# Optimization experiments

Hardware: AMD Instinct MI355X
Metric: run time of the kernel (lower is better)

The kernel has to match this reference:

```python
import jax, jax.numpy as jnp
import numpy as np

DIM = 1024
DIM_INNER = 1536  # int(1024 * 1.5)


def _log_g(x):
    # log of g(x) = where(x>=0, x+0.5, sigmoid(x)) computed stably in log-space
    return jnp.where(x >= 0.0, jnp.log(jnp.maximum(x, 0.0) + 0.5), -jax.nn.softplus(-x))


def _heinsen_scan_log(log_coefficients, log_values):
    # parallel associative scan in log space over the sequence axis (axis=1)
    a_star = jnp.cumsum(log_coefficients, axis=1)
    log_h0_plus_b_star = jax.lax.cumlogsumexp(log_values - a_star, axis=1)
    return jnp.exp(a_star + log_h0_plus_b_star)


def _forward_gru(x, W_hg, W_out):
    # x: [b, s, dim] -> hidden/gate: [b, s, dim_inner]
    hg = jnp.einsum('bsd,ed->bse', x, W_hg)
    hidden, gate = jnp.split(hg, 2, axis=-1)
    log_coefficients = -jax.nn.softplus(gate)      # log(1 - z)
    log_z = -jax.nn.softplus(-gate)                # log z
    log_values = log_z + _log_g(hidden)
    out = _heinsen_scan_log(log_coefficients, log_values)  # [b, s, dim_inner]
    return jnp.einsum('bse,de->bsd', out, W_out)


def setup_inputs() -> dict:
    key = jax.random.key(0)
    k1, k2, k3 = jax.random.split(key, 3)
    x = jax.random.normal(k1, (4, 4096, DIM), dtype=jnp.float32)
    W_hg = jax.random.normal(k2, (2 * DIM_INNER, DIM), dtype=jnp.float32) * (DIM ** -0.5)
    W_out = jax.random.normal(k3, (DIM, DIM_INNER), dtype=jnp.float32) * (DIM_INNER ** -0.5)
    return {"x": x, "W_hg": W_hg, "W_out": W_out}


def reference(x, W_hg, W_out):
    out_forward = _forward_gru(x, W_hg, W_out)
    # bidirectional=True: run on time-flipped input and add (module does NOT flip back)
    out_backward = _forward_gru(jnp.flip(x, axis=1), W_hg, W_out)
    return out_forward + out_backward
```

## Files before the change

kernel.cpp:

```cpp
#include <hip/hip_runtime.h>
#include <hip/hip_fp16.h>
#include <cstdint>
#include <cstddef>

#define B_ 4
#define S_ 4096
#define D_ 1024
#define E_ 1536
#define M_ (B_*S_)
#define BE_ (B_*E_)
#define C_ 32
#define L_ (S_/C_)

typedef short bf16x8 __attribute__((ext_vector_type(8)));
typedef float f32x4 __attribute__((ext_vector_type(4)));

__device__ __forceinline__ unsigned short f2b(float f) {
  union { float f; unsigned int i; } x; x.f = f;
  unsigned int r = x.i + 0x7FFFu + ((x.i >> 16) & 1u);
  return (unsigned short)(r >> 16);
}
__device__ __forceinline__ float h2f(unsigned short u) { return __half2float(__ushort_as_half(u)); }
__device__ __forceinline__ unsigned int packcv(float c, float v) {
  return (unsigned int)__half_as_ushort(__float2half_rn(c)) |
         ((unsigned int)__half_as_ushort(__float2half_rn(v)) << 16);
}

__global__ __launch_bounds__(256) void cvt_bf16(const float* __restrict__ src,
                                                unsigned short* __restrict__ dst) {
  const int i = blockIdx.x * 256 + threadIdx.x;
  float4 f = ((const float4*)src)[i];
  ushort4 u; u.x = f2b(f.x); u.y = f2b(f.y); u.z = f2b(f.z); u.w = f2b(f.w);
  ((ushort4*)dst)[i] = u;
}

__global__ __launch_bounds__(256) void gemm1_mfma(const unsigned short* __restrict__ Xb,
                                                  const unsigned short* __restrict__ Wb,
                                                  unsigned int* __restrict__ CV) {
  __shared__ unsigned short lA[128 * 32];
  __shared__ unsigned short lB[128 * 32];
  const int t = threadIdx.x;
  const int m0 = blockIdx.x * 128;
  const int n0 = blockIdx.y * 64;
  const int wv = t >> 6, lane = t & 63;
  const int wm = wv >> 1, we = wv & 1;
  const int lm = lane & 15, kg = lane >> 4;
  const int r1 = t >> 2, q1 = t & 3;
  const int r2 = r1 + 64;
  const int gb1 = (r1 < 64) ? (n0 + r1) : (E_ + n0 + r1 - 64);
  const int gb2 = (r2 < 64) ? (n0 + r2) : (E_ + n0 + r2 - 64);

  const f32x4 z4 = {0.f, 0.f, 0.f, 0.f};
  f32x4 ah[4][2], ag[4][2];
#pragma unroll
  for (int i = 0; i < 4; ++i)
#pragma unroll
    for (int j = 0; j < 2; ++j) { ah[i][j] = z4; ag[i][j] = z4; }

  for (int k0 = 0; k0 < D_; k0 += 32) {
    *(uint4*)(lA + (size_t)r1 * 32 + q1 * 8) = *(const uint4*)(Xb + (size_t)(m0 + r1) * D_ + k0 + q1 * 8);
    *(uint4*)(lA + (size_t)r2 * 32 + q1 * 8) = *(const uint4*)(Xb + (size_t)(m0 + r2) * D_ + k0 + q1 * 8);
    *(uint4*)(lB + (size_t)r1 * 32 + q1 * 8) = *(const uint4*)(Wb + (size_t)gb1 * D_ + k0 + q1 * 8);
    *(uint4*)(lB + (size_t)r2 * 32 + q1 * 8) = *(const uint4*)(Wb + (size_t)gb2 * D_ + k0 + q1 * 8);
    __syncthreads();
    bf16x8 af[4], bh[2], bg[2];
#pragma unroll
    for (int mt = 0; mt < 4; ++mt)
      af[mt] = *(const bf16x8*)(lA + (size_t)(wm * 64 + mt * 16 + lm) * 32 + kg * 8);
#pragma unroll
    for (int et = 0; et < 2; ++et) {
      bh[et] = *(const bf16x8*)(lB + (size_t)(we * 32 + et * 16 + lm) * 32 + kg * 8);
      bg[et] = *(const bf16x8*)(lB + (size_t)(64 + we * 32 + et * 16 + lm) * 32 + kg * 8);
    }
#pragma unroll
    for (int mt = 0; mt < 4; ++mt)
#pragma unroll
      for (int et = 0; et < 2; ++et) {
        ah[mt][et] = __builtin_amdgcn_mfma_f32_16x16x32_bf16(af[mt], bh[et], ah[mt][et], 0, 0, 0);
        ag[mt][et] = __builtin_amdgcn_mfma_f32_16x16x32_bf16(af[mt], bg[et], ag[mt][et], 0, 0, 0);
      }
    __syncthreads();
  }
#pragma unroll
  for (int mt = 0; mt < 4; ++mt)
#pragma unroll
    for (int et = 0; et < 2; ++et) {
      const int e = n0 + we * 32 + et * 16 + lm;
#pragma unroll
      for (int r = 0; r < 4; ++r) {
        const int m = m0 + wm * 64 + mt * 16 + kg * 4 + r;
        const float hid = ah[mt][et][r];
        const float gat = ag[mt][et][r];
        const float z = 1.f / (1.f + expf(-gat));
        const float c = 1.f / (1.f + expf(gat));
        const float gv = (hid >= 0.f) ? (hid + 0.5f) : (1.f / (1.f + expf(-hid)));
        CV[(size_t)m * E_ + e] = packcv(c, z * gv);
      }
    }
}

__global__ __launch_bounds__(256) void scan_p1(const unsigned int* __restrict__ CV,
                                               float* __restrict__ P, float* __restrict__ Qf,
                                               float* __restrict__ Qr) {
  const int be = blockIdx.x * 256 + threadIdx.x;
  const int b = be / E_, e = be - b * E_;
  const int k = blockIdx.y;
  const unsigned int* cv = CV + (size_t)b * S_ * E_ + e + (size_t)k * L_ * E_;
  float pp = 1.f, qf = 0.f, qr = 0.f;
  for (int l = 0; l < L_; ++l) {
    const unsigned int p = cv[(size_t)l * E_];
    const float c = h2f((unsigned short)p), v = h2f((unsigned short)(p >> 16));
    qf = fmaf(c, qf, v);
    qr = fmaf(pp, v, qr);
    pp *= c;
  }
  P[(size_t)k * BE_ + be] = pp;
  Qf[(size_t)k * BE_ + be] = qf;
  Qr[(size_t)k * BE_ + be] = qr;
}

__global__ __launch_bounds__(256) void scan_p2(const float* __restrict__ P, const float* __restrict__ Qf,
                                               const float* __restrict__ Qr, float* __restrict__ HfIn,
                                               float* __restrict__ HbIn) {
  const int be = blockIdx.x * 256 + threadIdx.x;
  float hf = 0.f;
  for (int k = 0; k < C_; ++k) {
    HfIn[(size_t)k * BE_ + be] = hf;
    hf = fmaf(P[(size_t)k * BE_ + be], hf, Qf[(size_t)k * BE_ + be]);
  }
  float hb = 0.f;
  for (int k = C_ - 1; k >= 0; --k) {
    HbIn[(size_t)k * BE_ + be] = hb;
    hb = fmaf(P[(size_t)k * BE_ + be], hb, Qr[(size_t)k * BE_ + be]);
  }
}

__global__ __launch_bounds__(256) void scan_p3(const unsigned int* __restrict__ CV,
                                               const float* __restrict__ HfIn,
                                               const float* __restrict__ HbIn,
                                               unsigned short* __restrict__ Hb) {
  const int be = blockIdx.x * 256 + threadIdx.x;
  const int b = be / E_, e = be - b * E_;
  const int k = blockIdx.y;
  const unsigned int* cv = CV + (size_t)b * S_ * E_ + e;
  const unsigned int* cvf = cv + (size_t)k * L_ * E_;
  const unsigned int* cvb = cv + (size_t)(S_ - 1 - k * L_) * E_;
  unsigned short* hp = Hb + (size_t)b * S_ * E_ + e + (size_t)k * L_ * E_;
  float hf = HfIn[(size_t)k * BE_ + be];
  float hb = HbIn[(size_t)(C_ - 1 - k) * BE_ + be];
  for (int l = 0; l < L_; ++l) {
    const unsigned int pf = cvf[(size_t)l * E_];
    const unsigned int pb = *(cvb - (ptrdiff_t)l * E_);
    hf = fmaf(h2f((unsigned short)pf), hf, h2f((unsigned short)(pf >> 16)));
    hb = fmaf(h2f((unsigned short)pb), hb, h2f((unsigned short)(pb >> 16)));
    hp[(size_t)l * E_] = f2b(hf + hb);
  }
}

__global__ __launch_bounds__(256) void gemm2_mfma(const unsigned short* __restrict__ Hb,
                                                  const unsigned short* __restrict__ Wob,
                                                  float* __restrict__ Out) {
  __shared__ unsigned short lA[128 * 32];
  __shared__ unsigned short lB[128 * 32];
  const int t = threadIdx.x;
  const int m0 = blockIdx.x * 128;
  const int n0 = blockIdx.y * 128;
  const int wv = t >> 6, lane = t & 63;
  const int wm = wv >> 1, wn = wv & 1;
  const int lm = lane & 15, kg = lane >> 4;
  const int r1 = t >> 2, q1 = t & 3;
  const int r2 = r1 + 64;

  const f32x4 z4 = {0.f, 0.f, 0.f, 0.f};
  f32x4 acc[4][4];
#pragma unroll
  for (int i = 0; i < 4; ++i)
#pragma unroll
    for (int j = 0; j < 4; ++j) acc[i][j] = z4;

  for (int k0 = 0; k0 < E_; k0 += 32) {
    *(uint4*)(lA + (size_t)r1 * 32 + q1 * 8) = *(const uint4*)(Hb + (size_t)(m0 + r1) * E_ + k0 + q1 * 8);
    *(uint4*)(lA + (size_t)r2 * 32 + q1 * 8) = *(const uint4*)(Hb + (size_t)(m0 + r2) * E_ + k0 + q1 * 8);
    *(uint4*)(lB + (size_t)r1 * 32 + q1 * 8) = *(const uint4*)(Wob + (size_t)(n0 + r1) * E_ + k0 + q1 * 8);
    *(uint4*)(lB + (size_t)r2 * 32 + q1 * 8) = *(const uint4*)(Wob + (size_t)(n0 + r2) * E_ + k0 + q1 * 8);
    __syncthreads();
    bf16x8 af[4], bf[4];
#pragma unroll
    for (int mt = 0; mt < 4; ++mt)
      af[mt] = *(const bf16x8*)(lA + (size_t)(wm * 64 + mt * 16 + lm) * 32 + kg * 8);
#pragma unroll
    for (int nt = 0; nt < 4; ++nt)
      bf[nt] = *(const bf16x8*)(lB + (size_t)(wn * 64 + nt * 16 + lm) * 32 + kg * 8);
#pragma unroll
    for (int mt = 0; mt < 4; ++mt)
#pragma unroll
      for (int nt = 0; nt < 4; ++nt)
        acc[mt][nt] = __builtin_amdgcn_mfma_f32_16x16x32_bf16(af[mt], bf[nt], acc[mt][nt], 0, 0, 0);
    __syncthreads();
  }
#pragma unroll
  for (int mt = 0; mt < 4; ++mt)
#pragma unroll
    for (int nt = 0; nt < 4; ++nt) {
      const int d = n0 + wn * 64 + nt * 16 + lm;
#pragma unroll
      for (int r = 0; r < 4; ++r) {
        const int m = m0 + wm * 64 + mt * 16 + kg * 4 + r;
        Out[(size_t)m * D_ + d] = acc[mt][nt][r];
      }
    }
}

extern "C" void kernel_launch(void* const* d_in, const int* in_sizes, int n_in,
                              void* d_out, int out_size, void* d_ws, size_t ws_size,
                              hipStream_t stream) {
  const float* x    = (const float*)d_in[0];
  const float* whg  = (const float*)d_in[1];
  const float* wout = (const float*)d_in[2];
  float* out = (float*)d_out;

  unsigned int*  CV = (unsigned int*)d_ws;
  unsigned short* Hb = (unsigned short*)((char*)d_ws + (size_t)M_ * E_ * 4);
  unsigned short* Xb  = Hb;
  unsigned short* Wb  = Xb + (size_t)M_ * D_;
  unsigned short* Wob = (unsigned short*)d_ws;
  float* P    = out;
  float* Qf   = out + (size_t)C_ * BE_;
  float* Qr   = out + 2 * (size_t)C_ * BE_;
  float* HfIn = out + 3 * (size_t)C_ * BE_;
  float* HbIn = out + 4 * (size_t)C_ * BE_;

  cvt_bf16<<<M_ * D_ / 1024, 256, 0, stream>>>(x, Xb);
  cvt_bf16<<<2 * E_ * D_ / 1024, 256, 0, stream>>>(whg, Wb);
  gemm1_mfma<<<dim3(M_ / 128, E_ / 64), 256, 0, stream>>>(Xb, Wb, CV);
  scan_p1<<<dim3(BE_ / 256, C_), 256, 0, stream>>>(CV, P, Qf, Qr);
  scan_p2<<<BE_ / 256, 256, 0, stream>>>(P, Qf, Qr, HfIn, HbIn);
  scan_p3<<<dim3(BE_ / 256, C_), 256, 0, stream>>>(CV, HfIn, HbIn, Hb);
  cvt_bf16<<<D_ * E_ / 1024, 256, 0, stream>>>(wout, Wob);
  gemm2_mfma<<<dim3(M_ / 128, D_ / 128), 256, 0, stream>>>(Hb, Wob, out);
}
```

Baseline: 416.9 us.

## Use direct global-to-LDS loads in GEMMs and vectorize scan passes by two

Both MFMA GEMMs now stage their A/B tiles through global_load_lds, which writes 16 bytes per lane straight into LDS and avoids routing the data through VGPRs. Each wave now loads whole 16-row chunks in the same row-major layout as before. The scan passes p1 and p3 now handle two channels per thread using uint2/float2 accesses with unroll 8, halving the grid and widening memory transactions. The risk is that the GEMMs still use one buffer with no double buffering, so load latency is not overlapped, and the wider scan threads give half as many wavefronts to hide memory latency.

```diff
diff --git a/kernel.cpp b/kernel.cpp
--- a/kernel.cpp
+++ b/kernel.cpp
@@ -24,6 +24,10 @@
 __device__ __forceinline__ unsigned int packcv(float c, float v) {
   return (unsigned int)__half_as_ushort(__float2half_rn(c)) |
          ((unsigned int)__half_as_ushort(__float2half_rn(v)) << 16);
+}
+__device__ __forceinline__ void async16(const unsigned short* g, unsigned short* l) {
+  __builtin_amdgcn_global_load_lds((const __attribute__((address_space(1))) unsigned int*)g,
+                                   (__attribute__((address_space(3))) unsigned int*)l, 16, 0, 0);
 }
 
 __global__ __launch_bounds__(256) void cvt_bf16(const float* __restrict__ src,
@@ -45,10 +49,7 @@
   const int wv = t >> 6, lane = t & 63;
   const int wm = wv >> 1, we = wv & 1;
   const int lm = lane & 15, kg = lane >> 4;
-  const int r1 = t >> 2, q1 = t & 3;
-  const int r2 = r1 + 64;
-  const int gb1 = (r1 < 64) ? (n0 + r1) : (E_ + n0 + r1 - 64);
-  const int gb2 = (r2 < 64) ? (n0 + r2) : (E_ + n0 + r2 - 64);
+  const int lrow = lane >> 2, lq = lane & 3;
 
   const f32x4 z4 = {0.f, 0.f, 0.f, 0.f};
   f32x4 ah[4][2], ag[4][2];
@@ -58,10 +59,18 @@
     for (int j = 0; j < 2; ++j) { ah[i][j] = z4; ag[i][j] = z4; }
 
   for (int k0 = 0; k0 < D_; k0 += 32) {
-    *(uint4*)(lA + (size_t)r1 * 32 + q1 * 8) = *(const uint4*)(Xb + (size_t)(m0 + r1) * D_ + k0 + q1 * 8);
-    *(uint4*)(lA + (size_t)r2 * 32 + q1 * 8) = *(const uint4*)(Xb + (size_t)(m0 + r2) * D_ + k0 + q1 * 8);
-    *(uint4*)(lB + (size_t)r1 * 32 + q1 * 8) = *(const uint4*)(Wb + (size_t)gb1 * D_ + k0 + q1 * 8);
-    *(uint4*)(lB + (size_t)r2 * 32 + q1 * 8) = *(const uint4*)(Wb + (size_t)gb2 * D_ + k0 + q1 * 8);
+#pragma unroll
+    for (int j = 0; j < 4; ++j) {
+      const int c = (wv << 2) | j;
+      if (c < 8) {
+        const int row = c * 16 + lrow;
+        async16(Xb + (size_t)(m0 + row) * D_ + k0 + lq * 8, lA + (size_t)c * 512);
+      } else {
+        const int row = (c - 8) * 16 + lrow;
+        const int gr = (row < 64) ? (n0 + row) : (E_ + n0 + row - 64);
+        async16(Wb + (size_t)gr * D_ + k0 + lq * 8, lB + (size_t)(c - 8) * 512);
+      }
+    }
     __syncthreads();
     bf16x8 af[4], bh[2], bg[2];
 #pragma unroll
@@ -99,24 +108,27 @@
     }
 }
 
-__global__ __launch_bounds__(256) void scan_p1(const unsigned int* __restrict__ CV,
-                                               float* __restrict__ P, float* __restrict__ Qf,
-                                               float* __restrict__ Qr) {
-  const int be = blockIdx.x * 256 + threadIdx.x;
-  const int b = be / E_, e = be - b * E_;
+__global__ __launch_bounds__(256) void scan_p1(const uint2* __restrict__ CV2,
+                                               float2* __restrict__ P2, float2* __restrict__ Qf2,
+                                               float2* __restrict__ Qr2) {
+  const int pe = blockIdx.x * 256 + threadIdx.x;
+  const int b = pe / (E_ / 2), e2 = pe - b * (E_ / 2);
   const int k = blockIdx.y;
-  const unsigned int* cv = CV + (size_t)b * S_ * E_ + e + (size_t)k * L_ * E_;
-  float pp = 1.f, qf = 0.f, qr = 0.f;
+  const uint2* cv = CV2 + ((size_t)b * S_ + (size_t)k * L_) * (E_ / 2) + e2;
+  float pp0 = 1.f, qf0 = 0.f, qr0 = 0.f;
+  float pp1 = 1.f, qf1 = 0.f, qr1 = 0.f;
+#pragma unroll 8
   for (int l = 0; l < L_; ++l) {
-    const unsigned int p = cv[(size_t)l * E_];
-    const float c = h2f((unsigned short)p), v = h2f((unsigned short)(p >> 16));
-    qf = fmaf(c, qf, v);
-    qr = fmaf(pp, v, qr);
-    pp *= c;
-  }
-  P[(size_t)k * BE_ + be] = pp;
-  Qf[(size_t)k * BE_ + be] = qf;
-  Qr[(size_t)k * BE_ + be] = qr;
+    const uint2 p = cv[(size_t)l * (E_ / 2)];
+    const float c0 = h2f((unsigned short)p.x), v0 = h2f((unsigned short)(p.x >> 16));
+    const float c1 = h2f((unsigned short)p.y), v1 = h2f((unsigned short)(p.y >> 16));
+    qf0 = fmaf(c0, qf0, v0); qr0 = fmaf(pp0, v0, qr0); pp0 *= c0;
+    qf1 = fmaf(c1, qf1, v1); qr1 = fmaf(pp1, v1, qr1); pp1 *= c1;
+  }
+  const size_t o = (size_t)k * (BE_ / 2) + pe;
+  P2[o]  = make_float2(pp0, pp1);
+  Qf2[o] = make_float2(qf0, qf1);
+  Qr2[o] = make_float2(qr0, qr1);
 }
 
 __global__ __launch_bounds__(256) void scan_p2(const float* __restrict__ P, const float* __restrict__ Qf,
@@ -135,25 +147,28 @@
   }
 }
 
-__global__ __launch_bounds__(256) void scan_p3(const unsigned int* __restrict__ CV,
-                                               const float* __restrict__ HfIn,
-                                               const float* __restrict__ HbIn,
-                                               unsigned short* __restrict__ Hb) {
-  const int be = blockIdx.x * 256 + threadIdx.x;
-  const int b = be / E_, e = be - b * E_;
+__global__ __launch_bounds__(256) void scan_p3(const uint2* __restrict__ CV2,
+                                               const float2* __restrict__ HfIn2,
+                                               const float2* __restrict__ HbIn2,
+                                               unsigned int* __restrict__ Hb2) {
+  const int pe = blockIdx.x * 256 + threadIdx.x;
+  const int b = pe / (E_ / 2), e2 = pe - b * (E_ / 2);
   const int k = blockIdx.y;
-  const unsigned int* cv = CV + (size_t)b * S_ * E_ + e;
-  const unsigned int* cvf = cv + (size_t)k * L_ * E_;
-  const unsigned int* cvb = cv + (size_t)(S_ - 1 - k * L_) * E_;
-  unsigned short* hp = Hb + (size_t)b * S_ * E_ + e + (size_t)k * L_ * E_;
-  float hf = HfIn[(size_t)k * BE_ + be];
-  float hb = HbIn[(size_t)(C_ - 1 - k) * BE_ + be];
+  const uint2* cvf = CV2 + ((size_t)b * S_ + (size_t)k * L_) * (E_ / 2) + e2;
+  const uint2* cvb = CV2 + ((size_t)b * S_ + (size_t)(S_ - 1 - k * L_)) * (E_ / 2) + e2;
+  unsigned int* hp = Hb2 + ((size_t)b * S_ + (size_t)k * L_) * (E_ / 2) + e2;
+  const float2 f0 = HfIn2[(size_t)k * (BE_ / 2) + pe];
+  const float2 b0 = HbIn2[(size_t)(C_ - 1 - k) * (BE_ / 2) + pe];
+  float hf0 = f0.x, hf1 = f0.y, hb0 = b0.x, hb1 = b0.y;
+#pragma unroll 8
   for (int l = 0; l < L_; ++l) {
-    const unsigned int pf = cvf[(size_t)l * E_];
-    const unsigned int pb = *(cvb - (ptrdiff_t)l * E_);
-    hf = fmaf(h2f((unsigned short)pf), hf, h2f((unsigned short)(pf >> 16)));
-    hb = fmaf(h2f((unsigned short)pb), hb, h2f((unsigned short)(pb >> 16)));
-    hp[(size_t)l * E_] = f2b(hf + hb);
+    const uint2 pf = cvf[(size_t)l * (E_ / 2)];
+    const uint2 pb = *(cvb - (ptrdiff_t)l * (E_ / 2));
+    hf0 = fmaf(h2f((unsigned short)pf.x), hf0, h2f((unsigned short)(pf.x >> 16)));
+    hf1 = fmaf(h2f((unsigned short)pf.y), hf1, h2f((unsigned short)(pf.y >> 16)));
+    hb0 = fmaf(h2f((unsigned short)pb.x), hb0, h2f((unsigned short)(pb.x >> 16)));
+    hb1 = fmaf(h2f((unsigned short)pb.y), hb1, h2f((unsigned short)(pb.y >> 16)));
+    hp[(size_t)l * (E_ / 2)] = (unsigned int)f2b(hf0 + hb0) | ((unsigned int)f2b(hf1 + hb1) << 16);
   }
 }
 
@@ -168,8 +183,7 @@
   const int wv = t >> 6, lane = t & 63;
   const int wm = wv >> 1, wn = wv & 1;
   const int lm = lane & 15, kg = lane >> 4;
-  const int r1 = t >> 2, q1 = t & 3;
-  const int r2 = r1 + 64;
+  const int lrow = lane >> 2, lq = lane & 3;
 
   const f32x4 z4 = {0.f, 0.f, 0.f, 0.f};
   f32x4 acc[4][4];
@@ -179,10 +193,17 @@
     for (int j = 0; j < 4; ++j) acc[i][j] = z4;
 
   for (int k0 = 0; k0 < E_; k0 += 32) {
-    *(uint4*)(lA + (size_t)r1 * 32 + q1 * 8) = *(const uint4*)(Hb + (size_t)(m0 + r1) * E_ + k0 + q1 * 8);
-    *(uint4*)(lA + (size_t)r2 * 32 + q1 * 8) = *(const uint4*)(Hb + (size_t)(m0 + r2) * E_ + k0 + q1 * 8);
-    *(uint4*)(lB + (size_t)r1 * 32 + q1 * 8) = *(const uint4*)(Wob + (size_t)(n0 + r1) * E_ + k0 + q1 * 8);
-    *(uint4*)(lB + (size_t)r2 * 32 + q1 * 8) = *(const uint4*)(Wob + (size_t)(n0 + r2) * E_ + k0 + q1 * 8);
+#pragma unroll
+    for (int j = 0; j < 4; ++j) {
+      const int c = (wv << 2) | j;
+      if (c < 8) {
+        const int row = c * 16 + lrow;
+        async16(Hb + (size_t)(m0 + row) * E_ + k0 + lq * 8, lA + (size_t)c * 512);
+      } else {
+        const int row = (c - 8) * 16 + lrow;
+        async16(Wob + (size_t)(n0 + row) * E_ + k0 + lq * 8, lB + (size_t)(c - 8) * 512);
+      }
+    }
     __syncthreads();
     bf16x8 af[4], bf[4];
 #pragma unroll
@@ -233,9 +254,10 @@
   cvt_bf16<<<M_ * D_ / 1024, 256, 0, stream>>>(x, Xb);
   cvt_bf16<<<2 * E_ * D_ / 1024, 256, 0, stream>>>(whg, Wb);
   gemm1_mfma<<<dim3(M_ / 128, E_ / 64), 256, 0, stream>>>(Xb, Wb, CV);
-  scan_p1<<<dim3(BE_ / 256, C_), 256, 0, stream>>>(CV, P, Qf, Qr);
+  scan_p1<<<dim3(BE_ / 512, C_), 256, 0, stream>>>((const uint2*)CV, (float2*)P, (float2*)Qf, (float2*)Qr);
   scan_p2<<<BE_ / 256, 256, 0, stream>>>(P, Qf, Qr, HfIn, HbIn);
-  scan_p3<<<dim3(BE_ / 256, C_), 256, 0, stream>>>(CV, HfIn, HbIn, Hb);
+  scan_p3<<<dim3(BE_ / 512, C_), 256, 0, stream>>>((const uint2*)CV, (const float2*)HfIn,
+                                                   (const float2*)HbIn, (unsigned int*)Hb);
   cvt_bf16<<<D_ * E_ / 1024, 256, 0, stream>>>(wout, Wob);
   gemm2_mfma<<<dim3(M_ / 128, D_ / 128), 256, 0, stream>>>(Hb, Wob, out);
 }
```

Measured after the change: 443.9 us. +6.5%, slower.
